# Performance work log

Hardware: AMD Instinct MI355X
Metric: run time of the kernel (lower is better)

## Reference

```python
import jax, jax.numpy as jnp
import numpy as np

H, FFN, NH = 1024, 4096, 16
DK = H // NH
SCALE = DK ** -0.5


def _ln(x, g, b, eps=1e-5):
    m = jnp.mean(x, axis=-1, keepdims=True)
    v = jnp.var(x, axis=-1, keepdims=True)
    return (x - m) * jax.lax.rsqrt(v + eps) * g + b


def setup_inputs() -> dict:
    key = jax.random.key(0)
    ks = jax.random.split(key, 16)
    B, S = 4, 2048
    s = lambda fan: fan ** -0.5
    d = {
        "x": jax.random.normal(ks[0], (B, S, H), jnp.float32),
        "attn_bias": jax.random.normal(ks[1], (1, NH, S, S), jnp.float32),
        "ln1_g": jnp.ones((H,), jnp.float32),
        "ln1_b": jnp.zeros((H,), jnp.float32),
        "Wq": jax.random.normal(ks[2], (H, H), jnp.float32) * s(H),
        "bq": jnp.zeros((H,), jnp.float32),
        "Wk": jax.random.normal(ks[3], (H, H), jnp.float32) * s(H),
        "bk": jnp.zeros((H,), jnp.float32),
        "Wv": jax.random.normal(ks[4], (H, H), jnp.float32) * s(H),
        "bv": jnp.zeros((H,), jnp.float32),
        "Wo": jax.random.normal(ks[5], (H, H), jnp.float32) * s(H),
        "bo": jnp.zeros((H,), jnp.float32),
        "ln2_g": jnp.ones((H,), jnp.float32),
        "ln2_b": jnp.zeros((H,), jnp.float32),
        "W1": jax.random.normal(ks[6], (H, FFN), jnp.float32) * s(H),
        "b1": jnp.zeros((FFN,), jnp.float32),
        "W2": jax.random.normal(ks[7], (FFN, H), jnp.float32) * s(FFN),
        "b2": jnp.zeros((H,), jnp.float32),
    }
    return d


def reference(x, attn_bias, ln1_g, ln1_b, Wq, bq, Wk, bk, Wv, bv, Wo, bo,
              ln2_g, ln2_b, W1, b1, W2, b2):
    B, S, _ = x.shape
    y = _ln(x, ln1_g, ln1_b)
    q = (y @ Wq + bq).reshape(B, S, NH, DK)
    k = (y @ Wk + bk).reshape(B, S, NH, DK)
    v = (y @ Wv + bv).reshape(B, S, NH, DK)
    scores = jnp.einsum("bqhd,bkhd->bhqk", q * SCALE, k) + attn_bias
    A = jax.nn.softmax(scores, axis=-1)
    out = jnp.einsum("bhqk,bkhd->bqhd", A, v).reshape(B, S, H)
    x = x + (out @ Wo + bo)
    y = _ln(x, ln2_g, ln2_b)
    y = jax.nn.gelu(y @ W1 + b1, approximate=False) @ W2 + b2
    return x + y
```

## Files before the change

### kernel.cpp

```cpp
#include <hip/hip_runtime.h>

#define DEVINL __device__ __forceinline__

typedef __bf16 bf16x8 __attribute__((ext_vector_type(8)));
typedef float f32x4 __attribute__((ext_vector_type(4)));
typedef unsigned short ushort8_t __attribute__((ext_vector_type(8)));
typedef unsigned short u16x4 __attribute__((ext_vector_type(4)));

static constexpr int Bb = 4, S = 2048, H = 1024, NH = 16, DK = 64, FF = 4096;
static constexpr int Mrows = Bb * S;
static constexpr int QS = 3 * H;

DEVINL unsigned short f2bf(float f) {
    union { __bf16 b; unsigned short u; } r;
    r.b = (__bf16)f;
    return r.u;
}

DEVINL unsigned pack_bf2(float a, float b) {
    union { __bf16 h[2]; unsigned u; } r;
    r.h[0] = (__bf16)a; r.h[1] = (__bf16)b;
    return r.u;
}

DEVINL void gld16(const void* g, void* l) {
    auto gp = reinterpret_cast<const __attribute__((address_space(1))) unsigned*>(
        reinterpret_cast<unsigned long long>(g));
    auto lp = reinterpret_cast<__attribute__((address_space(3))) unsigned*>(
        (unsigned)reinterpret_cast<unsigned long long>(l));
    __builtin_amdgcn_global_load_lds(gp, lp, 16, 0, 0);
}

__global__ __launch_bounds__(256)
void wcvt(const float* __restrict__ in, unsigned short* __restrict__ out, int K, int N) {
    __shared__ float t[32][33];
    int n0 = blockIdx.x * 32, k0 = blockIdx.y * 32;
    int tx = threadIdx.x, ty = threadIdx.y;
#pragma unroll
    for (int i = 0; i < 32; i += 8) t[ty + i][tx] = in[(size_t)(k0 + ty + i) * N + n0 + tx];
    __syncthreads();
#pragma unroll
    for (int i = 0; i < 32; i += 8) out[(size_t)(n0 + ty + i) * K + k0 + tx] = f2bf(t[tx][ty + i]);
}

__global__ __launch_bounds__(256)
void catbias(const float* __restrict__ a, const float* __restrict__ b,
             const float* __restrict__ c, float* __restrict__ o) {
    int i = blockIdx.x * 256 + threadIdx.x;
    float v = (i < 1024) ? a[i] : (i < 2048 ? b[i - 1024] : c[i - 2048]);
    o[i] = v;
}

__global__ __launch_bounds__(256)
void ln_kernel(const float* __restrict__ x, const float* __restrict__ g,
               const float* __restrict__ be, unsigned short* __restrict__ y) {
    int row = blockIdx.x, tid = threadIdx.x;
    const float4 v = ((const float4*)(x + (size_t)row * H))[tid];
    float s = v.x + v.y + v.z + v.w;
    float ss = v.x * v.x + v.y * v.y + v.z * v.z + v.w * v.w;
#pragma unroll
    for (int m = 1; m < 64; m <<= 1) { s += __shfl_xor(s, m); ss += __shfl_xor(ss, m); }
    __shared__ float red[2][4];
    int lane = tid & 63, w = tid >> 6;
    if (lane == 0) { red[0][w] = s; red[1][w] = ss; }
    __syncthreads();
    s = red[0][0] + red[0][1] + red[0][2] + red[0][3];
    ss = red[1][0] + red[1][1] + red[1][2] + red[1][3];
    float mean = s * (1.f / H);
    float var = ss * (1.f / H) - mean * mean;
    float rstd = rsqrtf(var + 1e-5f);
    float4 gv = ((const float4*)g)[tid];
    float4 bv = ((const float4*)be)[tid];
    ushort4 o;
    o.x = f2bf((v.x - mean) * rstd * gv.x + bv.x);
    o.y = f2bf((v.y - mean) * rstd * gv.y + bv.y);
    o.z = f2bf((v.z - mean) * rstd * gv.z + bv.z);
    o.w = f2bf((v.w - mean) * rstd * gv.w + bv.w);
    ((ushort4*)(y + (size_t)row * H))[tid] = o;
}

template <int EPI>
__global__ __launch_bounds__(256)
void gemm_kernel(const unsigned short* __restrict__ A, const unsigned short* __restrict__ Bt,
                 const float* __restrict__ bias, const float* __restrict__ resid,
                 void* __restrict__ outp, int M, int N, int K) {
    __shared__ __align__(16) unsigned short lA[128 * 32];
    __shared__ __align__(16) unsigned short lB[128 * 32];
    const int tid = threadIdx.x;
    const int lane = tid & 63, w = tid >> 6;
    const int wr = w >> 1, wc = w & 1;
    const int m0 = blockIdx.x * 128, n0 = blockIdx.y * 128;
    const int fr = lane & 15, fq = lane >> 4;
    f32x4 acc[4][4] = {};

    const int srow = (w * 2) * 16 + (lane >> 2);
    const int scol = (lane & 3) * 8;
    const size_t abase = (size_t)(m0 + srow) * K + scol;
    const size_t bbase = (size_t)(n0 + srow) * K + scol;
    unsigned short* lA0 = &lA[(w * 2) * 16 * 32];
    unsigned short* lB0 = &lB[(w * 2) * 16 * 32];

    for (int k0 = 0; k0 < K; k0 += 32) {
        gld16(A + abase + k0, lA0);
        gld16(A + abase + (size_t)16 * K + k0, lA0 + 16 * 32);
        gld16(Bt + bbase + k0, lB0);
        gld16(Bt + bbase + (size_t)16 * K + k0, lB0 + 16 * 32);
        __syncthreads();
        bf16x8 af[4], bfr[4];
#pragma unroll
        for (int m = 0; m < 4; ++m) af[m] = *(const bf16x8*)&lA[(wr * 64 + m * 16 + fr) * 32 + fq * 8];
#pragma unroll
        for (int n = 0; n < 4; ++n) bfr[n] = *(const bf16x8*)&lB[(wc * 64 + n * 16 + fr) * 32 + fq * 8];
#pragma unroll
        for (int m = 0; m < 4; ++m)
#pragma unroll
            for (int n = 0; n < 4; ++n)
                acc[m][n] = __builtin_amdgcn_mfma_f32_16x16x32_bf16(af[m], bfr[n], acc[m][n], 0, 0, 0);
        __syncthreads();
    }

#pragma unroll
    for (int m = 0; m < 4; ++m) {
        int row0 = m0 + wr * 64 + m * 16 + fq * 4;
#pragma unroll
        for (int n = 0; n < 4; ++n) {
            int col = n0 + wc * 64 + n * 16 + fr;
            float bz = bias[col];
#pragma unroll
            for (int j = 0; j < 4; ++j) {
                float vv = acc[m][n][j] + bz;
                size_t idx = (size_t)(row0 + j) * N + col;
                if (EPI == 0) {
                    ((unsigned short*)outp)[idx] = f2bf(vv);
                } else if (EPI == 1) {
                    float t = 0.5f * vv * (1.f + erff(vv * 0.70710678118654752f));
                    ((unsigned short*)outp)[idx] = f2bf(t);
                } else {
                    ((float*)outp)[idx] = vv + resid[idx];
                }
            }
        }
    }
}

template <int EPI>
__global__ __launch_bounds__(512, 2)
void gemm8p(const unsigned short* __restrict__ A, const unsigned short* __restrict__ Bt,
            const float* __restrict__ bias, void* __restrict__ outp, int N, int K) {
    __shared__ __align__(16) char lds[131072];
    const int tid = threadIdx.x, lane = tid & 63, w = tid >> 6;
    const int wm = w >> 2, wn = w & 3;
    const int fr = lane & 15, fq = lane >> 4;
    const int nwg = gridDim.x, id = blockIdx.x;
    const int swz = (id & 7) * (nwg >> 3) + (id >> 3);
    const int m0 = (swz & 31) * 256, n0 = (swz >> 5) * 256;

    int srow[2], scol[2];
#pragma unroll
    for (int l = 0; l < 2; ++l) {
        int idx = l * 512 + tid;
        srow[l] = idx >> 3;
        scol[l] = ((idx & 7) ^ (srow[l] & 7)) * 8;
    }
    const int NT = K >> 6;

    auto stage = [&](int ht, int buf, int kt) {
        const unsigned short* src = (ht < 2) ? A : Bt;
        const int hh = ht & 1;
        char* dst = lds + ((ht < 2 ? 0 : 65536) + (buf * 2 + hh) * 16384);
        const int rbase = ((ht < 2) ? m0 : n0) + hh * 128;
        const int kb = kt * 64;
#pragma unroll
        for (int l = 0; l < 2; ++l)
            gld16(src + (size_t)(rbase + srow[l]) * K + kb + scol[l],
                  dst + (size_t)(l * 512 + tid) * 16);
    };

    int oa[2];
#pragma unroll
    for (int ks = 0; ks < 2; ++ks)
        oa[ks] = fr * 128 + (((ks * 4 + fq) ^ (fr & 7)) & 7) * 16;
    const int aBase0 = wm * 16384;
    const int bBase0 = 65536 + (wn >> 1) * 16384 + (wn & 1) * 8192;

    f32x4 acc[8][4] = {};
    bf16x8 aF[4][2], bF[4][2];

    stage(0, 0, 0); stage(1, 0, 0); stage(2, 0, 0); stage(3, 0, 0);
    if (NT > 1) {
        stage(0, 1, 1);
        asm volatile("s_waitcnt vmcnt(2)" ::: "memory");
    } else {
        asm volatile("s_waitcnt vmcnt(0)" ::: "memory");
    }
    __builtin_amdgcn_s_barrier();

    int buf = 0;
    for (int t = 0; t < NT; ++t, buf ^= 1) {
        const char* Ar = lds + aBase0 + buf * 32768;
        const char* Br = lds + bBase0 + buf * 32768;

#pragma unroll
        for (int mb = 0; mb < 4; ++mb)
#pragma unroll
            for (int ks = 0; ks < 2; ++ks)
                aF[mb][ks] = *(const bf16x8*)(Ar + mb * 2048 + oa[ks]);
#pragma unroll
        for (int nb = 0; nb < 2; ++nb)
#pragma unroll
            for (int ks = 0; ks < 2; ++ks)
                bF[nb][ks] = *(const bf16x8*)(Br + nb * 2048 + oa[ks]);
        if (t + 1 < NT) stage(1, buf ^ 1, t + 1);
        __builtin_amdgcn_s_barrier();
        asm volatile("s_waitcnt lgkmcnt(0)" ::: "memory");
        __builtin_amdgcn_sched_barrier(0);
        __builtin_amdgcn_s_setprio(1);
#pragma unroll
        for (int mb = 0; mb < 4; ++mb)
#pragma unroll
            for (int nb = 0; nb < 2; ++nb)
#pragma unroll
                for (int ks = 0; ks < 2; ++ks)
                    acc[mb][nb] = __builtin_amdgcn_mfma_f32_16x16x32_bf16(aF[mb][ks], bF[nb][ks], acc[mb][nb], 0, 0, 0);
        __builtin_amdgcn_s_setprio(0);
        __builtin_amdgcn_s_barrier();

#pragma unroll
        for (int nb = 2; nb < 4; ++nb)
#pragma unroll
            for (int ks = 0; ks < 2; ++ks)
                bF[nb][ks] = *(const bf16x8*)(Br + nb * 2048 + oa[ks]);
        if (t + 1 < NT) stage(2, buf ^ 1, t + 1);
        __builtin_amdgcn_s_barrier();
        asm volatile("s_waitcnt lgkmcnt(0)" ::: "memory");
        __builtin_amdgcn_sched_barrier(0);
        __builtin_amdgcn_s_setprio(1);
#pragma unroll
        for (int mb = 0; mb < 4; ++mb)
#pragma unroll
            for (int nb = 2; nb < 4; ++nb)
#pragma unroll
                for (int ks = 0; ks < 2; ++ks)
                    acc[mb][nb] = __builtin_amdgcn_mfma_f32_16x16x32_bf16(aF[mb][ks], bF[nb][ks], acc[mb][nb], 0, 0, 0);
        __builtin_amdgcn_s_setprio(0);
        __builtin_amdgcn_s_barrier();

#pragma unroll
        for (int mb = 0; mb < 4; ++mb)
#pragma unroll
            for (int ks = 0; ks < 2; ++ks)
                aF[mb][ks] = *(const bf16x8*)(Ar + 8192 + mb * 2048 + oa[ks]);
        if (t + 1 < NT) stage(3, buf ^ 1, t + 1);
        __builtin_amdgcn_s_barrier();
        asm volatile("s_waitcnt lgkmcnt(0)" ::: "memory");
        __builtin_amdgcn_sched_barrier(0);
        __builtin_amdgcn_s_setprio(1);
#pragma unroll
        for (int mb = 0; mb < 4; ++mb)
#pragma unroll
            for (int nb = 0; nb < 2; ++nb)
#pragma unroll
                for (int ks = 0; ks < 2; ++ks)
                    acc[4 + mb][nb] = __builtin_amdgcn_mfma_f32_16x16x32_bf16(aF[mb][ks], bF[nb][ks], acc[4 + mb][nb], 0, 0, 0);
        __builtin_amdgcn_s_setprio(0);
        __builtin_amdgcn_s_barrier();

        if (t + 2 < NT) {
            stage(0, buf, t + 2);
            asm volatile("s_waitcnt vmcnt(2)" ::: "memory");
        } else if (t + 1 < NT) {
            asm volatile("s_waitcnt vmcnt(0)" ::: "memory");
        }
        __builtin_amdgcn_s_barrier();
        __builtin_amdgcn_s_setprio(1);
#pragma unroll
        for (int mb = 0; mb < 4; ++mb)
#pragma unroll
            for (int nb = 2; nb < 4; ++nb)
#pragma unroll
                for (int ks = 0; ks < 2; ++ks)
                    acc[4 + mb][nb] = __builtin_amdgcn_mfma_f32_16x16x32_bf16(aF[mb][ks], bF[nb][ks], acc[4 + mb][nb], 0, 0, 0);
        __builtin_amdgcn_s_setprio(0);
        __builtin_amdgcn_s_barrier();
    }

#pragma unroll
    for (int mb = 0; mb < 8; ++mb) {
        int row0 = m0 + wm * 128 + mb * 16 + fq * 4;
#pragma unroll
        for (int nb = 0; nb < 4; ++nb) {
            int col = n0 + wn * 64 + nb * 16 + fr;
            float bz = bias[col];
#pragma unroll
            for (int j = 0; j < 4; ++j) {
                float vv = acc[mb][nb][j] + bz;
                size_t idx = (size_t)(row0 + j) * N + col;
                if (EPI == 0) {
                    ((unsigned short*)outp)[idx] = f2bf(vv);
                } else {
                    float tg = 0.5f * vv * (1.f + erff(vv * 0.70710678118654752f));
                    ((unsigned short*)outp)[idx] = f2bf(tg);
                }
            }
        }
    }
}

__global__ __launch_bounds__(256)
void attn_kernel(const unsigned short* __restrict__ QKV, const float* __restrict__ bias,
                 unsigned short* __restrict__ O) {
    __shared__ __align__(16) unsigned short lK[2][4096];
    __shared__ __align__(16) unsigned short lV[2][4096];
    __shared__ __align__(16) unsigned short lP[4][1024];
    const int tid = threadIdx.x, lane = tid & 63, w = tid >> 6;
    const int fr = lane & 15, fq = lane >> 4;

    const int bid = blockIdx.x;
    const int slice = (bid >> 5) * 8 + (bid & 7);
    const int b = (bid >> 3) & 3;
    const int h = slice >> 5;
    const int q0 = (slice & 31) * 64;

    const size_t base = (size_t)b * S * QS + h * DK;
    const unsigned short* Qp = QKV + base;
    const unsigned short* Kp = QKV + base + H;
    const unsigned short* Vp = QKV + base + 2 * H;
    const size_t obase = (size_t)b * S * H + h * DK;

    bf16x8 aq[2];
    {
        const unsigned short* qp = Qp + (size_t)(q0 + w * 16 + fr) * QS + fq * 8;
        aq[0] = *(const bf16x8*)qp;
        aq[1] = *(const bf16x8*)(qp + 32);
    }

    const int chk0 = w * 128 + lane, chk1 = chk0 + 64;
    const int rK0 = chk0 >> 3, cK0 = ((chk0 & 7) ^ (rK0 & 7)) * 8;
    const int rK1 = chk1 >> 3, cK1 = ((chk1 & 7) ^ (rK1 & 7)) * 8;
    int vk0, vd0, vk1, vd1;
    {
        int ch = chk0;
        int dch = ch & 1, j = (ch >> 1) & 3, fqi = (ch >> 3) & 3, half = (ch >> 5) & 1,
            c = (ch >> 6) & 3, ks = (ch >> 8) & 1;
        vk0 = ks * 32 + fqi * 8 + half * 4 + j; vd0 = c * 16 + dch * 8;
        ch = chk1;
        dch = ch & 1; j = (ch >> 1) & 3; fqi = (ch >> 3) & 3; half = (ch >> 5) & 1;
        c = (ch >> 6) & 3; ks = (ch >> 8) & 1;
        vk1 = ks * 32 + fqi * 8 + half * 4 + j; vd1 = c * 16 + dch * 8;
    }

    f32x4 oacc[4] = {};
    float mrun = -3e38f, lrun = 0.f;
    const float* bias_q = bias + (size_t)h * S * S + (size_t)(q0 + w * 16 + fr) * S;

    auto stage = [&](int buf, int k0) {
        gld16(Kp + (size_t)(k0 + rK0) * QS + cK0, &lK[buf][w * 1024]);
        gld16(Kp + (size_t)(k0 + rK1) * QS + cK1, &lK[buf][w * 1024 + 512]);
        gld16(Vp + (size_t)(k0 + vk0) * QS + vd0, &lV[buf][w * 1024]);
        gld16(Vp + (size_t)(k0 + vk1) * QS + vd1, &lV[buf][w * 1024 + 512]);
    };

    stage(0, 0);
    int cur = 0;
    for (int kt = 0; kt < S / 64; ++kt) {
        const int k0 = kt * 64;
        __syncthreads();
        if (kt + 1 < S / 64) stage(cur ^ 1, k0 + 64);

        float4 bv4[4];
#pragma unroll
        for (int c = 0; c < 4; ++c)
            bv4[c] = *(const float4*)(bias_q + k0 + c * 16 + fq * 4);

        f32x4 sacc[4] = {};
        __builtin_amdgcn_s_setprio(1);
#pragma unroll
        for (int c = 0; c < 4; ++c) {
            int row = c * 16 + fr;
#pragma unroll
            for (int dh = 0; dh < 2; ++dh) {
                bf16x8 bk = *(const bf16x8*)((char*)lK[cur] +
                    ((row * 128 + dh * 64 + fq * 16) ^ ((row & 7) << 4)));
                sacc[c] = __builtin_amdgcn_mfma_f32_16x16x32_bf16(bk, aq[dh], sacc[c], 0, 0, 0);
            }
        }
        __builtin_amdgcn_s_setprio(0);

        float p[4][4];
        float tmax = -3e38f;
#pragma unroll
        for (int c = 0; c < 4; ++c) {
            p[c][0] = fmaf(sacc[c][0], 0.125f, bv4[c].x);
            p[c][1] = fmaf(sacc[c][1], 0.125f, bv4[c].y);
            p[c][2] = fmaf(sacc[c][2], 0.125f, bv4[c].z);
            p[c][3] = fmaf(sacc[c][3], 0.125f, bv4[c].w);
#pragma unroll
            for (int j = 0; j < 4; ++j) tmax = fmaxf(tmax, p[c][j]);
        }
        tmax = fmaxf(tmax, __shfl_xor(tmax, 16));
        tmax = fmaxf(tmax, __shfl_xor(tmax, 32));

        float mnew = fmaxf(mrun, tmax);
        float sf = __expf(mrun - mnew);
        mrun = mnew;

        float rs = 0.f;
#pragma unroll
        for (int c = 0; c < 4; ++c)
#pragma unroll
            for (int j = 0; j < 4; ++j) {
                float pv = __expf(p[c][j] - mrun);
                p[c][j] = pv;
                rs += pv;
            }
        rs += __shfl_xor(rs, 16);
        rs += __shfl_xor(rs, 32);
        lrun = lrun * sf + rs;

        float sfo[4];
#pragma unroll
        for (int j = 0; j < 4; ++j) sfo[j] = __shfl(sf, fq * 4 + j);
#pragma unroll
        for (int c = 0; c < 4; ++c)
#pragma unroll
            for (int j = 0; j < 4; ++j) oacc[c][j] *= sfo[j];

#pragma unroll
        for (int c = 0; c < 4; ++c) {
            uint2 pk;
            pk.x = pack_bf2(p[c][0], p[c][1]);
            pk.y = pack_bf2(p[c][2], p[c][3]);
            *(uint2*)((char*)&lP[w][0] +
                ((fr * 128 + c * 32 + fq * 8) ^ ((fr & 7) << 4))) = pk;
        }

#pragma unroll
        for (int ks = 0; ks < 2; ++ks) {
            bf16x8 pa = *(const bf16x8*)((char*)&lP[w][0] +
                ((fr * 128 + ks * 64 + fq * 16) ^ ((fr & 7) << 4)));
            const char* vb8 = (const char*)lV[cur] + ks * 4096;
            u16x4 ra[4], rb[4];
#pragma unroll
            for (int c = 0; c < 4; ++c) {
                unsigned ad = (unsigned)(unsigned long long)(vb8 + c * 1024) + lane * 8;
                asm volatile("ds_read_b64_tr_b16 %0, %1" : "=&v"(ra[c]) : "v"(ad));
                asm volatile("ds_read_b64_tr_b16 %0, %1 offset:512" : "=&v"(rb[c]) : "v"(ad));
            }
            asm volatile("s_waitcnt lgkmcnt(0)" ::: "memory");
            __builtin_amdgcn_sched_barrier(0);
            __builtin_amdgcn_s_setprio(1);
#pragma unroll
            for (int c = 0; c < 4; ++c) {
                union { u16x4 h2[2]; bf16x8 v8; } u;
                u.h2[0] = ra[c]; u.h2[1] = rb[c];
                oacc[c] = __builtin_amdgcn_mfma_f32_16x16x32_bf16(pa, u.v8, oacc[c], 0, 0, 0);
            }
            __builtin_amdgcn_s_setprio(0);
        }
        cur ^= 1;
    }

    float linv = 1.f / lrun;
    float lo[4];
#pragma unroll
    for (int j = 0; j < 4; ++j) lo[j] = __shfl(linv, fq * 4 + j);
#pragma unroll
    for (int c = 0; c < 4; ++c)
#pragma unroll
        for (int j = 0; j < 4; ++j) {
            int row = q0 + w * 16 + fq * 4 + j;
            int d = c * 16 + fr;
            O[obase + (size_t)row * H + d] = f2bf(oacc[c][j] * lo[j]);
        }
}

extern "C" void kernel_launch(void* const* d_in, const int* in_sizes, int n_in,
                              void* d_out, int out_size, void* d_ws, size_t ws_size,
                              hipStream_t stream) {
    const float* x    = (const float*)d_in[0];
    const float* ab   = (const float*)d_in[1];
    const float* ln1g = (const float*)d_in[2];
    const float* ln1b = (const float*)d_in[3];
    const float* Wq   = (const float*)d_in[4];
    const float* bq   = (const float*)d_in[5];
    const float* Wk   = (const float*)d_in[6];
    const float* bk   = (const float*)d_in[7];
    const float* Wv   = (const float*)d_in[8];
    const float* bv   = (const float*)d_in[9];
    const float* Wo   = (const float*)d_in[10];
    const float* bo   = (const float*)d_in[11];
    const float* ln2g = (const float*)d_in[12];
    const float* ln2b = (const float*)d_in[13];
    const float* W1   = (const float*)d_in[14];
    const float* b1   = (const float*)d_in[15];
    const float* W2   = (const float*)d_in[16];
    const float* b2   = (const float*)d_in[17];

    char* ws = (char*)d_ws;
    size_t off = 0;
    auto alloc = [&](size_t bytes) -> void* {
        void* p = ws + off;
        off += (bytes + 255) & ~(size_t)255;
        return p;
    };
    unsigned short* Wqt = (unsigned short*)alloc((size_t)H * H * 2);
    unsigned short* Wkt = (unsigned short*)alloc((size_t)H * H * 2);
    unsigned short* Wvt = (unsigned short*)alloc((size_t)H * H * 2);
    unsigned short* Wot = (unsigned short*)alloc((size_t)H * H * 2);
    unsigned short* W1t = (unsigned short*)alloc((size_t)H * FF * 2);
    unsigned short* W2t = (unsigned short*)alloc((size_t)H * FF * 2);
    float* bqkv        = (float*)alloc((size_t)QS * 4);
    unsigned short* ybuf = (unsigned short*)alloc((size_t)Mrows * H * 2);
    unsigned short* qkvb = (unsigned short*)alloc((size_t)Mrows * QS * 2);
    unsigned short* ob = (unsigned short*)alloc((size_t)Mrows * H * 2);
    unsigned short* hb = (unsigned short*)alloc((size_t)Mrows * FF * 2);
    (void)ws_size; (void)in_sizes; (void)n_in; (void)out_size;

    dim3 tb(32, 8, 1);
    wcvt<<<dim3(H / 32, H / 32), tb, 0, stream>>>(Wq, Wqt, H, H);
    wcvt<<<dim3(H / 32, H / 32), tb, 0, stream>>>(Wk, Wkt, H, H);
    wcvt<<<dim3(H / 32, H / 32), tb, 0, stream>>>(Wv, Wvt, H, H);
    wcvt<<<dim3(H / 32, H / 32), tb, 0, stream>>>(Wo, Wot, H, H);
    wcvt<<<dim3(FF / 32, H / 32), tb, 0, stream>>>(W1, W1t, H, FF);
    wcvt<<<dim3(H / 32, FF / 32), tb, 0, stream>>>(W2, W2t, FF, H);
    catbias<<<QS / 256, 256, 0, stream>>>(bq, bk, bv, bqkv);

    ln_kernel<<<Mrows, 256, 0, stream>>>(x, ln1g, ln1b, ybuf);

    gemm8p<0><<<dim3((Mrows / 256) * (QS / 256)), 512, 0, stream>>>(ybuf, Wqt, bqkv, qkvb, QS, H);

    attn_kernel<<<dim3(Bb * NH * (S / 64)), 256, 0, stream>>>(qkvb, ab, ob);

    gemm_kernel<2><<<dim3(Mrows / 128, H / 128), 256, 0, stream>>>(ob, Wot, bo, x, d_out, Mrows, H, H);

    ln_kernel<<<Mrows, 256, 0, stream>>>((const float*)d_out, ln2g, ln2b, ybuf);

    gemm8p<1><<<dim3((Mrows / 256) * (FF / 256)), 512, 0, stream>>>(ybuf, W1t, b1, hb, FF, H);

    gemm_kernel<2><<<dim3(Mrows / 128, H / 128), 256, 0, stream>>>(hb, W2t, b2, (const float*)d_out, d_out, Mrows, H, FF);
}
```

Baseline: 602.2 us.

## Replace N=1024 GEMMs with pipelined 128x256 kernel; widen attention blocks, shuffle P

Drops the simple single-buffered 128x128 GEMM used for the Wo and W2 projections and adds a double-buffered, swizzled 128x256-tile, 8-wave kernel with a fused bias+residual epilogue. This cuts the LDS stalls and low MFMA utilisation of the old kernel. Attention blocks grow to 8 waves covering 128 queries, so each K/V tile staged in LDS serves more queries. The P matrix now reaches the PV MFMA through lane shuffles instead of an LDS round trip. The risks are register pressure from launch bounds (512,8) on attention and correctness of the new shuffle mapping and tile-index math.

Measured after the change: 840.9 us. 39.6% more time.

```diff
diff --git a/kernel.cpp b/kernel.cpp
--- a/kernel.cpp
+++ b/kernel.cpp
@@ -4,7 +4,6 @@
 
 typedef __bf16 bf16x8 __attribute__((ext_vector_type(8)));
 typedef float f32x4 __attribute__((ext_vector_type(4)));
-typedef unsigned short ushort8_t __attribute__((ext_vector_type(8)));
 typedef unsigned short u16x4 __attribute__((ext_vector_type(4)));
 
 static constexpr int Bb = 4, S = 2048, H = 1024, NH = 16, DK = 64, FF = 4096;
@@ -80,70 +79,6 @@
 }
 
 template <int EPI>
-__global__ __launch_bounds__(256)
-void gemm_kernel(const unsigned short* __restrict__ A, const unsigned short* __restrict__ Bt,
-                 const float* __restrict__ bias, const float* __restrict__ resid,
-                 void* __restrict__ outp, int M, int N, int K) {
-    __shared__ __align__(16) unsigned short lA[128 * 32];
-    __shared__ __align__(16) unsigned short lB[128 * 32];
-    const int tid = threadIdx.x;
-    const int lane = tid & 63, w = tid >> 6;
-    const int wr = w >> 1, wc = w & 1;
-    const int m0 = blockIdx.x * 128, n0 = blockIdx.y * 128;
-    const int fr = lane & 15, fq = lane >> 4;
-    f32x4 acc[4][4] = {};
-
-    const int srow = (w * 2) * 16 + (lane >> 2);
-    const int scol = (lane & 3) * 8;
-    const size_t abase = (size_t)(m0 + srow) * K + scol;
-    const size_t bbase = (size_t)(n0 + srow) * K + scol;
-    unsigned short* lA0 = &lA[(w * 2) * 16 * 32];
-    unsigned short* lB0 = &lB[(w * 2) * 16 * 32];
-
-    for (int k0 = 0; k0 < K; k0 += 32) {
-        gld16(A + abase + k0, lA0);
-        gld16(A + abase + (size_t)16 * K + k0, lA0 + 16 * 32);
-        gld16(Bt + bbase + k0, lB0);
-        gld16(Bt + bbase + (size_t)16 * K + k0, lB0 + 16 * 32);
-        __syncthreads();
-        bf16x8 af[4], bfr[4];
-#pragma unroll
-        for (int m = 0; m < 4; ++m) af[m] = *(const bf16x8*)&lA[(wr * 64 + m * 16 + fr) * 32 + fq * 8];
-#pragma unroll
-        for (int n = 0; n < 4; ++n) bfr[n] = *(const bf16x8*)&lB[(wc * 64 + n * 16 + fr) * 32 + fq * 8];
-#pragma unroll
-        for (int m = 0; m < 4; ++m)
-#pragma unroll
-            for (int n = 0; n < 4; ++n)
-                acc[m][n] = __builtin_amdgcn_mfma_f32_16x16x32_bf16(af[m], bfr[n], acc[m][n], 0, 0, 0);
-        __syncthreads();
-    }
-
-#pragma unroll
-    for (int m = 0; m < 4; ++m) {
-        int row0 = m0 + wr * 64 + m * 16 + fq * 4;
-#pragma unroll
-        for (int n = 0; n < 4; ++n) {
-            int col = n0 + wc * 64 + n * 16 + fr;
-            float bz = bias[col];
-#pragma unroll
-            for (int j = 0; j < 4; ++j) {
-                float vv = acc[m][n][j] + bz;
-                size_t idx = (size_t)(row0 + j) * N + col;
-                if (EPI == 0) {
-                    ((unsigned short*)outp)[idx] = f2bf(vv);
-                } else if (EPI == 1) {
-                    float t = 0.5f * vv * (1.f + erff(vv * 0.70710678118654752f));
-                    ((unsigned short*)outp)[idx] = f2bf(t);
-                } else {
-                    ((float*)outp)[idx] = vv + resid[idx];
-                }
-            }
-        }
-    }
-}
-
-template <int EPI>
 __global__ __launch_bounds__(512, 2)
 void gemm8p(const unsigned short* __restrict__ A, const unsigned short* __restrict__ Bt,
             const float* __restrict__ bias, void* __restrict__ outp, int N, int K) {
@@ -306,20 +241,180 @@
     }
 }
 
-__global__ __launch_bounds__(256)
+__global__ __launch_bounds__(512, 2)
+void gemm8p128(const unsigned short* __restrict__ A, const unsigned short* __restrict__ Bt,
+               const float* __restrict__ bias, const float* __restrict__ resid,
+               float* __restrict__ outp, int N, int K) {
+    __shared__ __align__(16) char lds[98304];
+    const int tid = threadIdx.x, lane = tid & 63, w = tid >> 6;
+    const int wm = w >> 2, wn = w & 3;
+    const int fr = lane & 15, fq = lane >> 4;
+    const int nwg = gridDim.x, id = blockIdx.x;
+    const int swz = (id & 7) * (nwg >> 3) + (id >> 3);
+    const int m0 = (swz & 63) * 128, n0 = (swz >> 6) * 256;
+
+    int srow[2], scol[2];
+#pragma unroll
+    for (int l = 0; l < 2; ++l) {
+        int idx = l * 512 + tid;
+        srow[l] = idx >> 3;
+        scol[l] = ((idx & 7) ^ (srow[l] & 7)) * 8;
+    }
+    const int NT = K >> 6;
+
+    auto stageA = [&](int buf, int kt) {
+        char* dst = lds + buf * 16384;
+#pragma unroll
+        for (int l = 0; l < 2; ++l)
+            gld16(A + (size_t)(m0 + srow[l]) * K + kt * 64 + scol[l],
+                  dst + (size_t)(l * 512 + tid) * 16);
+    };
+    auto stageB = [&](int hh, int buf, int kt) {
+        char* dst = lds + 32768 + buf * 32768 + hh * 16384;
+#pragma unroll
+        for (int l = 0; l < 2; ++l)
+            gld16(Bt + (size_t)(n0 + hh * 128 + srow[l]) * K + kt * 64 + scol[l],
+                  dst + (size_t)(l * 512 + tid) * 16);
+    };
+
+    int oa[2], ob[2];
+#pragma unroll
+    for (int ks = 0; ks < 2; ++ks) {
+        oa[ks] = fr * 128 + (((ks * 4 + fq) ^ (fr & 7)) & 7) * 16;
+        ob[ks] = fr * 128 + (((ks * 4 + fq) ^ (fr & 7)) & 7) * 16;
+    }
+    const int aWB = wm * 8192;
+    const int bWB = (wn >> 1) * 16384 + (wn & 1) * 8192;
+
+    f32x4 acc[4][4] = {};
+    bf16x8 aF[2][2], bF[4][2];
+
+    stageA(0, 0); stageB(0, 0, 0); stageB(1, 0, 0);
+    if (NT > 1) {
+        stageA(1, 1);
+        asm volatile("s_waitcnt vmcnt(2)" ::: "memory");
+    } else {
+        asm volatile("s_waitcnt vmcnt(0)" ::: "memory");
+    }
+    __builtin_amdgcn_s_barrier();
+
+    int buf = 0;
+    for (int t = 0; t < NT; ++t, buf ^= 1) {
+        const char* Ar = lds + buf * 16384 + aWB;
+        const char* Br = lds + 32768 + buf * 32768 + bWB;
+
+#pragma unroll
+        for (int mb = 0; mb < 2; ++mb)
+#pragma unroll
+            for (int ks = 0; ks < 2; ++ks)
+                aF[mb][ks] = *(const bf16x8*)(Ar + mb * 2048 + oa[ks]);
+#pragma unroll
+        for (int nb = 0; nb < 2; ++nb)
+#pragma unroll
+            for (int ks = 0; ks < 2; ++ks)
+                bF[nb][ks] = *(const bf16x8*)(Br + nb * 2048 + ob[ks]);
+        if (t + 1 < NT) stageB(0, buf ^ 1, t + 1);
+        __builtin_amdgcn_s_barrier();
+        asm volatile("s_waitcnt lgkmcnt(0)" ::: "memory");
+        __builtin_amdgcn_sched_barrier(0);
+        __builtin_amdgcn_s_setprio(1);
+#pragma unroll
+        for (int mb = 0; mb < 2; ++mb)
+#pragma unroll
+            for (int nb = 0; nb < 2; ++nb)
+#pragma unroll
+                for (int ks = 0; ks < 2; ++ks)
+                    acc[mb][nb] = __builtin_amdgcn_mfma_f32_16x16x32_bf16(aF[mb][ks], bF[nb][ks], acc[mb][nb], 0, 0, 0);
+        __builtin_amdgcn_s_setprio(0);
+        __builtin_amdgcn_s_barrier();
+
+#pragma unroll
+        for (int nb = 2; nb < 4; ++nb)
+#pragma unroll
+            for (int ks = 0; ks < 2; ++ks)
+                bF[nb][ks] = *(const bf16x8*)(Br + nb * 2048 + ob[ks]);
+        if (t + 1 < NT) stageB(1, buf ^ 1, t + 1);
+        __builtin_amdgcn_s_barrier();
+        asm volatile("s_waitcnt lgkmcnt(0)" ::: "memory");
+        __builtin_amdgcn_sched_barrier(0);
+        __builtin_amdgcn_s_setprio(1);
+#pragma unroll
+        for (int mb = 0; mb < 2; ++mb)
+#pragma unroll
+            for (int nb = 2; nb < 4; ++nb)
+#pragma unroll
+                for (int ks = 0; ks < 2; ++ks)
+                    acc[mb][nb] = __builtin_amdgcn_mfma_f32_16x16x32_bf16(aF[mb][ks], bF[nb][ks], acc[mb][nb], 0, 0, 0);
+        __builtin_amdgcn_s_setprio(0);
+        __builtin_amdgcn_s_barrier();
+
+#pragma unroll
+        for (int mb = 0; mb < 2; ++mb)
+#pragma unroll
+            for (int ks = 0; ks < 2; ++ks)
+                aF[mb][ks] = *(const bf16x8*)(Ar + 4096 + mb * 2048 + oa[ks]);
+        __builtin_amdgcn_s_barrier();
+        asm volatile("s_waitcnt lgkmcnt(0)" ::: "memory");
+        __builtin_amdgcn_sched_barrier(0);
+        __builtin_amdgcn_s_setprio(1);
+#pragma unroll
+        for (int mb = 0; mb < 2; ++mb)
+#pragma unroll
+            for (int nb = 0; nb < 2; ++nb)
+#pragma unroll
+                for (int ks = 0; ks < 2; ++ks)
+                    acc[2 + mb][nb] = __builtin_amdgcn_mfma_f32_16x16x32_bf16(aF[mb][ks], bF[nb][ks], acc[2 + mb][nb], 0, 0, 0);
+        __builtin_amdgcn_s_setprio(0);
+        __builtin_amdgcn_s_barrier();
+
+        if (t + 2 < NT) {
+            stageA(buf, t + 2);
+            asm volatile("s_waitcnt vmcnt(2)" ::: "memory");
+        } else if (t + 1 < NT) {
+            asm volatile("s_waitcnt vmcnt(0)" ::: "memory");
+        }
+        __builtin_amdgcn_s_barrier();
+        __builtin_amdgcn_s_setprio(1);
+#pragma unroll
+        for (int mb = 0; mb < 2; ++mb)
+#pragma unroll
+            for (int nb = 2; nb < 4; ++nb)
+#pragma unroll
+                for (int ks = 0; ks < 2; ++ks)
+                    acc[2 + mb][nb] = __builtin_amdgcn_mfma_f32_16x16x32_bf16(aF[mb][ks], bF[nb][ks], acc[2 + mb][nb], 0, 0, 0);
+        __builtin_amdgcn_s_setprio(0);
+        __builtin_amdgcn_s_barrier();
+    }
+
+#pragma unroll
+    for (int mb = 0; mb < 4; ++mb) {
+        int row0 = m0 + wm * 64 + mb * 16 + fq * 4;
+#pragma unroll
+        for (int nb = 0; nb < 4; ++nb) {
+            int col = n0 + wn * 64 + nb * 16 + fr;
+            float bz = bias[col];
+#pragma unroll
+            for (int j = 0; j < 4; ++j) {
+                size_t idx = (size_t)(row0 + j) * N + col;
+                outp[idx] = acc[mb][nb][j] + bz + resid[idx];
+            }
+        }
+    }
+}
+
+__global__ __launch_bounds__(512, 8)
 void attn_kernel(const unsigned short* __restrict__ QKV, const float* __restrict__ bias,
                  unsigned short* __restrict__ O) {
     __shared__ __align__(16) unsigned short lK[2][4096];
     __shared__ __align__(16) unsigned short lV[2][4096];
-    __shared__ __align__(16) unsigned short lP[4][1024];
     const int tid = threadIdx.x, lane = tid & 63, w = tid >> 6;
     const int fr = lane & 15, fq = lane >> 4;
 
     const int bid = blockIdx.x;
     const int slice = (bid >> 5) * 8 + (bid & 7);
     const int b = (bid >> 3) & 3;
-    const int h = slice >> 5;
-    const int q0 = (slice & 31) * 64;
+    const int h = slice >> 4;
+    const int q0 = (slice & 15) * 128;
 
     const size_t base = (size_t)b * S * QS + h * DK;
     const unsigned short* Qp = QKV + base;
@@ -334,19 +429,14 @@
         aq[1] = *(const bf16x8*)(qp + 32);
     }
 
-    const int chk0 = w * 128 + lane, chk1 = chk0 + 64;
-    const int rK0 = chk0 >> 3, cK0 = ((chk0 & 7) ^ (rK0 & 7)) * 8;
-    const int rK1 = chk1 >> 3, cK1 = ((chk1 & 7) ^ (rK1 & 7)) * 8;
-    int vk0, vd0, vk1, vd1;
+    const int chk = w * 64 + lane;
+    const int rK = chk >> 3, cK = ((chk & 7) ^ (rK & 7)) * 8;
+    int vk, vd;
     {
-        int ch = chk0;
+        int ch = chk;
         int dch = ch & 1, j = (ch >> 1) & 3, fqi = (ch >> 3) & 3, half = (ch >> 5) & 1,
             c = (ch >> 6) & 3, ks = (ch >> 8) & 1;
-        vk0 = ks * 32 + fqi * 8 + half * 4 + j; vd0 = c * 16 + dch * 8;
-        ch = chk1;
-        dch = ch & 1; j = (ch >> 1) & 3; fqi = (ch >> 3) & 3; half = (ch >> 5) & 1;
-        c = (ch >> 6) & 3; ks = (ch >> 8) & 1;
-        vk1 = ks * 32 + fqi * 8 + half * 4 + j; vd1 = c * 16 + dch * 8;
+        vk = ks * 32 + fqi * 8 + half * 4 + j; vd = c * 16 + dch * 8;
     }
 
     f32x4 oacc[4] = {};
@@ -354,11 +444,12 @@
     const float* bias_q = bias + (size_t)h * S * S + (size_t)(q0 + w * 16 + fr) * S;
 
     auto stage = [&](int buf, int k0) {
-        gld16(Kp + (size_t)(k0 + rK0) * QS + cK0, &lK[buf][w * 1024]);
-        gld16(Kp + (size_t)(k0 + rK1) * QS + cK1, &lK[buf][w * 1024 + 512]);
-        gld16(Vp + (size_t)(k0 + vk0) * QS + vd0, &lV[buf][w * 1024]);
-        gld16(Vp + (size_t)(k0 + vk1) * QS + vd1, &lV[buf][w * 1024 + 512]);
+        gld16(Kp + (size_t)(k0 + rK) * QS + cK, &lK[buf][w * 512]);
+        gld16(Vp + (size_t)(k0 + vk) * QS + vd, &lV[buf][w * 512]);
     };
+
+    const int L0 = ((lane & 16) << 1) + fr;
+    const bool hisel = (lane & 32) != 0;
 
     stage(0, 0);
     int cur = 0;
@@ -425,19 +516,27 @@
 #pragma unroll
             for (int j = 0; j < 4; ++j) oacc[c][j] *= sfo[j];
 
+        unsigned pkx[4], pky[4];
 #pragma unroll
         for (int c = 0; c < 4; ++c) {
-            uint2 pk;
-            pk.x = pack_bf2(p[c][0], p[c][1]);
-            pk.y = pack_bf2(p[c][2], p[c][3]);
-            *(uint2*)((char*)&lP[w][0] +
-                ((fr * 128 + c * 32 + fq * 8) ^ ((fr & 7) << 4))) = pk;
+            pkx[c] = pack_bf2(p[c][0], p[c][1]);
+            pky[c] = pack_bf2(p[c][2], p[c][3]);
         }
 
 #pragma unroll
         for (int ks = 0; ks < 2; ++ks) {
-            bf16x8 pa = *(const bf16x8*)((char*)&lP[w][0] +
-                ((fr * 128 + ks * 64 + fq * 16) ^ ((fr & 7) << 4)));
+            unsigned lo0 = pkx[2 * ks], hi0 = pky[2 * ks];
+            unsigned lo1 = pkx[2 * ks + 1], hi1 = pky[2 * ks + 1];
+            unsigned a0 = __shfl(lo0, L0),      c0 = __shfl(lo1, L0);
+            unsigned a1 = __shfl(hi0, L0),      c1 = __shfl(hi1, L0);
+            unsigned a2 = __shfl(lo0, L0 + 16), c2 = __shfl(lo1, L0 + 16);
+            unsigned a3 = __shfl(hi0, L0 + 16), c3 = __shfl(hi1, L0 + 16);
+            union { unsigned u[4]; bf16x8 v; } pa;
+            pa.u[0] = hisel ? c0 : a0;
+            pa.u[1] = hisel ? c1 : a1;
+            pa.u[2] = hisel ? c2 : a2;
+            pa.u[3] = hisel ? c3 : a3;
+
             const char* vb8 = (const char*)lV[cur] + ks * 4096;
             u16x4 ra[4], rb[4];
 #pragma unroll
@@ -453,7 +552,7 @@
             for (int c = 0; c < 4; ++c) {
                 union { u16x4 h2[2]; bf16x8 v8; } u;
                 u.h2[0] = ra[c]; u.h2[1] = rb[c];
-                oacc[c] = __builtin_amdgcn_mfma_f32_16x16x32_bf16(pa, u.v8, oacc[c], 0, 0, 0);
+                oacc[c] = __builtin_amdgcn_mfma_f32_16x16x32_bf16(pa.v, u.v8, oacc[c], 0, 0, 0);
             }
             __builtin_amdgcn_s_setprio(0);
         }
@@ -515,6 +614,7 @@
     unsigned short* ob = (unsigned short*)alloc((size_t)Mrows * H * 2);
     unsigned short* hb = (unsigned short*)alloc((size_t)Mrows * FF * 2);
     (void)ws_size; (void)in_sizes; (void)n_in; (void)out_size;
+    (void)Wkt; (void)Wvt;
 
     dim3 tb(32, 8, 1);
     wcvt<<<dim3(H / 32, H / 32), tb, 0, stream>>>(Wq, Wqt, H, H);
@@ -529,13 +629,13 @@
 
     gemm8p<0><<<dim3((Mrows / 256) * (QS / 256)), 512, 0, stream>>>(ybuf, Wqt, bqkv, qkvb, QS, H);
 
-    attn_kernel<<<dim3(Bb * NH * (S / 64)), 256, 0, stream>>>(qkvb, ab, ob);
-
-    gemm_kernel<2><<<dim3(Mrows / 128, H / 128), 256, 0, stream>>>(ob, Wot, bo, x, d_out, Mrows, H, H);
+    attn_kernel<<<dim3(Bb * NH * (S / 128)), 512, 0, stream>>>(qkvb, ab, ob);
+
+    gemm8p128<<<dim3((Mrows / 128) * (H / 256)), 512, 0, stream>>>(ob, Wot, bo, x, (float*)d_out, H, H);
 
     ln_kernel<<<Mrows, 256, 0, stream>>>((const float*)d_out, ln2g, ln2b, ybuf);
 
     gemm8p<1><<<dim3((Mrows / 256) * (FF / 256)), 512, 0, stream>>>(ybuf, W1t, b1, hb, FF, H);
 
-    gemm_kernel<2><<<dim3(Mrows / 128, H / 128), 256, 0, stream>>>(hb, W2t, b2, (const float*)d_out, d_out, Mrows, H, FF);
-}
+    gemm8p128<<<dim3((Mrows / 128) * (H / 256)), 512, 0, stream>>>(hb, W2t, b2, (const float*)d_out, (float*)d_out, H, FF);
+}
```
